# Performance work log

Measured on AMD Instinct MI355X. Metric: run time of the kernel, lower is better.

Reference implementation:

```python
import jax, jax.numpy as jnp
import numpy as np

N_NODES = 10000
N_EDGES = 80000
OBS_DIMS = 128
HIDDEN = 1024
ACT_DIMS = 8
N_GRAPHS = 64


def setup_inputs() -> dict:
    key = jax.random.key(0)
    ks = jax.random.split(key, 8)
    x = jax.random.normal(ks[0], (N_NODES, OBS_DIMS), dtype=jnp.float32)
    edge_index = jax.random.randint(ks[1], (2, N_EDGES), 0, N_NODES, dtype=jnp.int64)
    batch = jnp.sort(jax.random.randint(ks[2], (N_NODES,), 0, N_GRAPHS, dtype=jnp.int64))
    # Glorot-style init for weights, zero bias (as in PyG GCNConv / Linear defaults)
    W1 = jax.random.normal(ks[3], (OBS_DIMS, HIDDEN), dtype=jnp.float32) * (1.0 / np.sqrt(OBS_DIMS))
    b1 = jnp.zeros((HIDDEN,), dtype=jnp.float32)
    W2 = jax.random.normal(ks[4], (HIDDEN, HIDDEN), dtype=jnp.float32) * (1.0 / np.sqrt(HIDDEN))
    b2 = jnp.zeros((HIDDEN,), dtype=jnp.float32)
    Wl = jax.random.normal(ks[5], (HIDDEN, ACT_DIMS), dtype=jnp.float32) * (1.0 / np.sqrt(HIDDEN))
    bl = jnp.zeros((ACT_DIMS,), dtype=jnp.float32)
    return {"x": x, "edge_index": edge_index, "batch": batch,
            "W1": W1, "b1": b1, "W2": W2, "b2": b2, "Wl": Wl, "bl": bl}


def _gcn_conv(x, src, dst, dinv, W, b, n):
    """PyG GCNConv: D^-1/2 (A+I) D^-1/2 X W + b (self-loops already in src/dst)."""
    h = x @ W                                   # [N, out]
    norm = (dinv[src] * dinv[dst])[:, None]      # [E+N, 1]
    msg = h[src] * norm                          # gather + scale
    out = jax.ops.segment_sum(msg, dst, num_segments=n)
    return out + b


def reference(x, edge_index, batch, W1, b1, W2, b2, Wl, bl):
    n = x.shape[0]
    loops = jnp.arange(n, dtype=edge_index.dtype)
    src = jnp.concatenate([edge_index[0], loops])  # add self-loops
    dst = jnp.concatenate([edge_index[1], loops])
    # degree (with self-loops) from destination column, as PyG does
    deg = jax.ops.segment_sum(jnp.ones_like(dst, dtype=x.dtype), dst, num_segments=n)
    dinv = jax.lax.rsqrt(jnp.maximum(deg, 1.0))

    h = jax.nn.relu(_gcn_conv(x, src, dst, dinv, W1, b1, n))
    h = _gcn_conv(h, src, dst, dinv, W2, b2, n)
    h = jnp.tanh(h @ Wl + bl)                    # [N, act_dims]

    # global_mean_pool over batch segment ids
    sums = jax.ops.segment_sum(h, batch, num_segments=N_GRAPHS)
    counts = jax.ops.segment_sum(jnp.ones((n, 1), h.dtype), batch, num_segments=N_GRAPHS)
    return sums / jnp.maximum(counts, 1.0)       # [N_GRAPHS, act_dims]
```

## Files before the change

kernel.cpp:

```cpp
#include <hip/hip_runtime.h>
#include <hip/hip_bf16.h>

#define NNODES 10000
#define NEDGES 80000
#define OBS    128
#define HID    1024
#define ACTD   8
#define NGR    64
#define CAP    32

typedef __bf16 bf16x8 __attribute__((ext_vector_type(8)));
typedef float  f32x4  __attribute__((ext_vector_type(4)));
typedef ushort us8    __attribute__((ext_vector_type(8)));
typedef const __attribute__((address_space(1))) unsigned int gl_u32;
typedef __attribute__((address_space(3))) unsigned int lds_u32;

__device__ __forceinline__ ushort f2b(float f) {
    union { float f; unsigned int i; } v; v.f = f;
    unsigned int lsb = (v.i >> 16) & 1u;
    unsigned int r = v.i + 0x7fffu + lsb;
    return (ushort)(r >> 16);
}
__device__ __forceinline__ int cix(int v, int hi) {
    return v < 0 ? 0 : (v >= hi ? hi - 1 : v);
}

__global__ __launch_bounds__(256) void k_fill(const int* __restrict__ src,
                                              const int* __restrict__ dst,
                                              const int* __restrict__ batch,
                                              int* __restrict__ deg,
                                              int* __restrict__ cntg,
                                              ushort* __restrict__ esrc,
                                              float* __restrict__ zacc,
                                              float* __restrict__ out) {
    __shared__ int lh[NGR];
    int t = threadIdx.x;
    int idx = blockIdx.x * 256 + t;
    if (t < NGR) lh[t] = 0;
    if (idx < NNODES * ACTD) zacc[idx] = 0.0f;
    if (idx < NGR * ACTD) out[idx] = 0.0f;
    if (idx < NEDGES) {
        int s = cix(src[idx], NNODES), d = cix(dst[idx], NNODES);
        int pos = atomicAdd(&deg[d], 1);
        if (pos < CAP) esrc[(size_t)d * CAP + pos] = (ushort)s;
    }
    __syncthreads();
    if (idx < NNODES) atomicAdd(&lh[cix(batch[idx], NGR)], 1);
    __syncthreads();
    if (t < NGR) {
        int c = lh[t];
        if (c) atomicAdd(&cntg[t], c);
    }
}

__global__ __launch_bounds__(256) void k_prepagg(const float* __restrict__ x,
                                                 const int* __restrict__ deg,
                                                 const ushort* __restrict__ esrc,
                                                 ushort* __restrict__ aggbf,
                                                 const float* __restrict__ W1,
                                                 const float* __restrict__ W2,
                                                 const float* __restrict__ Wl,
                                                 const float* __restrict__ b2,
                                                 const float* __restrict__ bl,
                                                 ushort* __restrict__ Wt1,
                                                 ushort* __restrict__ M2bf,
                                                 float* __restrict__ b2l) {
    int blk = blockIdx.x;
    int t = threadIdx.x;
    if (blk < 2500) {
        int wv = (blk * 256 + t) >> 6;
        int lane = t & 63;
        if (wv >= NNODES) return;
        int q = lane >> 4, c = lane & 15;
        int dg = deg[wv];
        float dd = rsqrtf((float)(dg + 1));
        float4 v0 = make_float4(0.f, 0.f, 0.f, 0.f), v1 = v0;
        if (q == 0) {
            const float* xs = x + (size_t)wv * OBS + c * 8;
            float4 a0 = *(const float4*)(xs);
            float4 a1 = *(const float4*)(xs + 4);
            v0.x = a0.x * dd; v0.y = a0.y * dd; v0.z = a0.z * dd; v0.w = a0.w * dd;
            v1.x = a1.x * dd; v1.y = a1.y * dd; v1.z = a1.z * dd; v1.w = a1.w * dd;
        }
        int dcl = dg < CAP ? dg : CAP;
        const ushort* bkt = esrc + (size_t)wv * CAP;
        for (int e = q; e < dcl; e += 4) {
            int s = bkt[e];
            float w = rsqrtf((float)(deg[s] + 1));
            const float* xs = x + (size_t)s * OBS + c * 8;
            float4 a0 = *(const float4*)(xs);
            float4 a1 = *(const float4*)(xs + 4);
            v0.x += a0.x * w; v0.y += a0.y * w; v0.z += a0.z * w; v0.w += a0.w * w;
            v1.x += a1.x * w; v1.y += a1.y * w; v1.z += a1.z * w; v1.w += a1.w * w;
        }
        #pragma unroll
        for (int off = 16; off <= 32; off <<= 1) {
            v0.x += __shfl_xor(v0.x, off); v0.y += __shfl_xor(v0.y, off);
            v0.z += __shfl_xor(v0.z, off); v0.w += __shfl_xor(v0.w, off);
            v1.x += __shfl_xor(v1.x, off); v1.y += __shfl_xor(v1.y, off);
            v1.z += __shfl_xor(v1.z, off); v1.w += __shfl_xor(v1.w, off);
        }
        if (q == 0) {
            us8 o;
            o[0] = f2b(v0.x * dd); o[1] = f2b(v0.y * dd); o[2] = f2b(v0.z * dd); o[3] = f2b(v0.w * dd);
            o[4] = f2b(v1.x * dd); o[5] = f2b(v1.y * dd); o[6] = f2b(v1.z * dd); o[7] = f2b(v1.w * dd);
            *(us8*)(aggbf + (size_t)wv * OBS + c * 8) = o;
        }
        return;
    }
    if (blk < 3525) {
        __shared__ float part[4][8];
        int r = blk - 2500;
        int lane = t & 63, w = t >> 6;
        const float* wrow = (r == HID) ? b2 : (W2 + (size_t)r * HID);
        float4 a = *((const float4*)wrow + t);
        float av[4] = {a.x, a.y, a.z, a.w};
        float acc[ACTD];
        #pragma unroll
        for (int j = 0; j < ACTD; ++j) acc[j] = 0.0f;
        #pragma unroll
        for (int kk = 0; kk < 4; ++kk) {
            int k = t * 4 + kk;
            float4 w0 = *(const float4*)(Wl + (size_t)k * ACTD);
            float4 w1 = *(const float4*)(Wl + (size_t)k * ACTD + 4);
            float av_k = av[kk];
            acc[0] += av_k * w0.x; acc[1] += av_k * w0.y;
            acc[2] += av_k * w0.z; acc[3] += av_k * w0.w;
            acc[4] += av_k * w1.x; acc[5] += av_k * w1.y;
            acc[6] += av_k * w1.z; acc[7] += av_k * w1.w;
        }
        #pragma unroll
        for (int off = 32; off > 0; off >>= 1)
            #pragma unroll
            for (int j = 0; j < ACTD; ++j)
                acc[j] += __shfl_down(acc[j], off);
        if (lane == 0)
            #pragma unroll
            for (int j = 0; j < ACTD; ++j) part[w][j] = acc[j];
        __syncthreads();
        if (t < ACTD) {
            float m = part[0][t] + part[1][t] + part[2][t] + part[3][t];
            if (r == HID) b2l[t] = m + bl[t];
            else          M2bf[r * ACTD + t] = f2b(m);
        }
        return;
    }
    __shared__ float tile[32][33];
    int tb = blk - 3525;
    int bx = (tb & 31) * 32, by = (tb >> 5) * 32;
    int tx = t & 31, ty = t >> 5;
    #pragma unroll
    for (int i = 0; i < 32; i += 8)
        tile[ty + i][tx] = W1[(size_t)(by + ty + i) * HID + bx + tx];
    __syncthreads();
    #pragma unroll
    for (int i = 0; i < 32; i += 8)
        Wt1[(size_t)(bx + ty + i) * OBS + by + tx] = f2b(tile[tx][ty + i]);
}

__global__ __launch_bounds__(256) void k_gemm1_fused(const ushort* __restrict__ A,
                                                     const ushort* __restrict__ Bt,
                                                     const float* __restrict__ bias,
                                                     const ushort* __restrict__ M2bf,
                                                     float* __restrict__ zacc,
                                                     int M) {
    __shared__ ushort buf[128 * 136 + 16 * 128];
    ushort* As    = buf;
    ushort* Bs    = buf + 8192;
    ushort* stage = buf;
    ushort* M2t   = buf + 128 * 136;

    const int t = threadIdx.x;
    const int bm = blockIdx.x, bn = blockIdx.y;
    const int lane = t & 63, wv = t >> 6;
    const int wm = (wv & 1) * 64, wn = (wv >> 1) * 64;
    const int l16 = lane & 15, kg = (lane >> 4) * 8;

    if (t < 128) {
        ushort4 a = *(const ushort4*)(M2bf + (size_t)(bn * 128 + t) * ACTD);
        ushort4 b = *(const ushort4*)(M2bf + (size_t)(bn * 128 + t) * ACTD + 4);
        M2t[0 * 128 + t] = a.x; M2t[1 * 128 + t] = a.y;
        M2t[2 * 128 + t] = a.z; M2t[3 * 128 + t] = a.w;
        M2t[4 * 128 + t] = b.x; M2t[5 * 128 + t] = b.y;
        M2t[6 * 128 + t] = b.z; M2t[7 * 128 + t] = b.w;
        #pragma unroll
        for (int j = 8; j < 16; ++j) M2t[j * 128 + t] = 0;
    }

    f32x4 acc[4][4];
    #pragma unroll
    for (int i = 0; i < 4; ++i)
        #pragma unroll
        for (int j = 0; j < 4; ++j)
            acc[i][j] = (f32x4){0.f, 0.f, 0.f, 0.f};

    const int rs = t >> 3;
    const int cs = (t & 7) * 8;
    #pragma unroll
    for (int kt = 0; kt < OBS; kt += 64) {
        #pragma unroll
        for (int p = 0; p < 4; ++p) {
            int r = rs + p * 32;
            int gr = bm * 128 + r; if (gr >= M) gr = M - 1;
            __builtin_amdgcn_global_load_lds(
                (gl_u32*)(A + (size_t)gr * OBS + kt + cs),
                (lds_u32*)(As + r * 64 + cs), 16, 0, 0);
            int gn = bn * 128 + r;
            __builtin_amdgcn_global_load_lds(
                (gl_u32*)(Bt + (size_t)gn * OBS + kt + cs),
                (lds_u32*)(Bs + r * 64 + cs), 16, 0, 0);
        }
        __syncthreads();
        #pragma unroll
        for (int k2 = 0; k2 < 64; k2 += 32) {
            bf16x8 af[4], bfr[4];
            #pragma unroll
            for (int i = 0; i < 4; ++i)
                af[i] = *(const bf16x8*)(As + (wm + i * 16 + l16) * 64 + k2 + kg);
            #pragma unroll
            for (int j = 0; j < 4; ++j)
                bfr[j] = *(const bf16x8*)(Bs + (wn + j * 16 + l16) * 64 + k2 + kg);
            #pragma unroll
            for (int i = 0; i < 4; ++i)
                #pragma unroll
                for (int j = 0; j < 4; ++j)
                    acc[i][j] = __builtin_amdgcn_mfma_f32_16x16x32_bf16(af[i], bfr[j], acc[i][j], 0, 0, 0);
        }
        __syncthreads();
    }

    #pragma unroll
    for (int i = 0; i < 4; ++i) {
        int rowb = wm + i * 16 + (lane >> 4) * 4;
        #pragma unroll
        for (int j = 0; j < 4; ++j) {
            int col = wn + j * 16 + l16;
            float bj = bias[bn * 128 + col];
            #pragma unroll
            for (int r = 0; r < 4; ++r)
                stage[(rowb + r) * 136 + col] = f2b(fmaxf(acc[i][j][r] + bj, 0.0f));
        }
    }
    __syncthreads();

    #pragma unroll
    for (int st = 0; st < 2; ++st) {
        int row0 = wv * 32 + st * 16;
        f32x4 z = (f32x4){0.f, 0.f, 0.f, 0.f};
        #pragma unroll
        for (int kt = 0; kt < 128; kt += 32) {
            bf16x8 a = *(const bf16x8*)(stage + (row0 + l16) * 136 + kt + kg);
            bf16x8 b = *(const bf16x8*)(M2t + l16 * 128 + kt + kg);
            z = __builtin_amdgcn_mfma_f32_16x16x32_bf16(a, b, z, 0, 0, 0);
        }
        if (l16 < ACTD) {
            int rowb = bm * 128 + row0 + (lane >> 4) * 4;
            #pragma unroll
            for (int r = 0; r < 4; ++r)
                if (rowb + r < M)
                    atomicAdd(&zacc[(size_t)(rowb + r) * ACTD + l16], z[r]);
        }
    }
}

__global__ __launch_bounds__(256) void k_zfinal(const float* __restrict__ zacc,
                                                const int* __restrict__ deg,
                                                const ushort* __restrict__ esrc,
                                                const float* __restrict__ b2l,
                                                const int* __restrict__ batch,
                                                const int* __restrict__ cntg,
                                                float* __restrict__ out, int n) {
    __shared__ float part[NGR * ACTD];
    int t = threadIdx.x;
    part[t] = 0.0f; part[t + 256] = 0.0f;
    __syncthreads();

    int idx = blockIdx.x * 256 + t;
    int i = idx >> 3, j = idx & 7;
    if (i < n) {
        int dg = deg[i];
        float dd = rsqrtf((float)(dg + 1));
        float v = dd * zacc[idx];
        int dcl = dg < CAP ? dg : CAP;
        const ushort* bkt = esrc + (size_t)i * CAP;
        for (int e = 0; e < dcl; ++e) {
            int s = bkt[e];
            float w = rsqrtf((float)(deg[s] + 1));
            v += w * zacc[(size_t)s * ACTD + j];
        }
        v *= dd;
        int g = cix(batch[i], NGR);
        int c = cntg[g];
        float invc = 1.0f / (float)(c > 0 ? c : 1);
        float tz = tanhf(v + b2l[j]) * invc;
        atomicAdd(&part[g * ACTD + j], tz);
    }
    __syncthreads();

    int i0 = (blockIdx.x * 256) >> 3;
    int i1 = (blockIdx.x * 256 + 255) >> 3;
    if (i0 >= n) return;
    if (i1 >= n) i1 = n - 1;
    int g0 = cix(batch[i0], NGR), g1 = cix(batch[i1], NGR);
    int ng = g1 - g0 + 1;
    for (int u = t; u < ng * ACTD; u += 256)
        atomicAdd(&out[g0 * ACTD + u], part[g0 * ACTD + u]);
}

extern "C" void kernel_launch(void* const* d_in, const int* in_sizes, int n_in,
                              void* d_out, int out_size, void* d_ws, size_t ws_size,
                              hipStream_t stream) {
    const float* x   = (const float*)d_in[0];
    const int*   ei  = (const int*)d_in[1];
    const int*   bat = (const int*)d_in[2];
    const float* W1  = (const float*)d_in[3];
    const float* b1  = (const float*)d_in[4];
    const float* W2  = (const float*)d_in[5];
    const float* b2v = (const float*)d_in[6];
    const float* Wl  = (const float*)d_in[7];
    const float* bl  = (const float*)d_in[8];
    float* out = (float*)d_out;

    const int N = NNODES, E = NEDGES;
    const int* src = ei;
    const int* dst = ei + E;

    char* ws = (char*)d_ws;
    size_t off = 0;
    int*    deg    = (int*)(ws + off);   off += 40192;
    int*    cntg   = (int*)(ws + off);   off += 256;
    float*  b2l    = (float*)(ws + off); off += 256;
    ushort* M2bf   = (ushort*)(ws + off); off += (size_t)HID * ACTD * 2;
    ushort* Wt1    = (ushort*)(ws + off); off += (size_t)HID * OBS * 2;
    float*  zacc   = (float*)(ws + off); off += (size_t)N * ACTD * 4;
    ushort* aggbf  = (ushort*)(ws + off); off += (size_t)N * OBS * 2;
    ushort* esrc   = (ushort*)(ws + off); off += (size_t)N * CAP * 2;

    hipMemsetAsync(deg, 0, 40448, stream);

    k_fill<<<313, 256, 0, stream>>>(src, dst, bat, deg, cntg, esrc, zacc, out);

    k_prepagg<<<3653, 256, 0, stream>>>(x, deg, esrc, aggbf,
                                        W1, W2, Wl, b2v, bl, Wt1, M2bf, b2l);

    k_gemm1_fused<<<dim3((N + 127) / 128, HID / 128), 256, 0, stream>>>(
        aggbf, Wt1, b1, M2bf, zacc, N);

    k_zfinal<<<(N * ACTD + 255) / 256, 256, 0, stream>>>(
        zacc, deg, esrc, b2l, bat, cntg, out, N);
}
```

Before: 113.2 us.

## Regroup launches: fuse weight prep into fill kernel, split aggregation, add ILP

```diff
diff --git a/kernel.cpp b/kernel.cpp
--- a/kernel.cpp
+++ b/kernel.cpp
@@ -25,92 +25,47 @@
     return v < 0 ? 0 : (v >= hi ? hi - 1 : v);
 }
 
-__global__ __launch_bounds__(256) void k_fill(const int* __restrict__ src,
-                                              const int* __restrict__ dst,
-                                              const int* __restrict__ batch,
-                                              int* __restrict__ deg,
-                                              int* __restrict__ cntg,
-                                              ushort* __restrict__ esrc,
-                                              float* __restrict__ zacc,
-                                              float* __restrict__ out) {
-    __shared__ int lh[NGR];
-    int t = threadIdx.x;
-    int idx = blockIdx.x * 256 + t;
-    if (t < NGR) lh[t] = 0;
-    if (idx < NNODES * ACTD) zacc[idx] = 0.0f;
-    if (idx < NGR * ACTD) out[idx] = 0.0f;
-    if (idx < NEDGES) {
-        int s = cix(src[idx], NNODES), d = cix(dst[idx], NNODES);
-        int pos = atomicAdd(&deg[d], 1);
-        if (pos < CAP) esrc[(size_t)d * CAP + pos] = (ushort)s;
-    }
-    __syncthreads();
-    if (idx < NNODES) atomicAdd(&lh[cix(batch[idx], NGR)], 1);
-    __syncthreads();
-    if (t < NGR) {
-        int c = lh[t];
-        if (c) atomicAdd(&cntg[t], c);
-    }
-}
-
-__global__ __launch_bounds__(256) void k_prepagg(const float* __restrict__ x,
-                                                 const int* __restrict__ deg,
-                                                 const ushort* __restrict__ esrc,
-                                                 ushort* __restrict__ aggbf,
-                                                 const float* __restrict__ W1,
-                                                 const float* __restrict__ W2,
-                                                 const float* __restrict__ Wl,
-                                                 const float* __restrict__ b2,
-                                                 const float* __restrict__ bl,
-                                                 ushort* __restrict__ Wt1,
-                                                 ushort* __restrict__ M2bf,
-                                                 float* __restrict__ b2l) {
+__global__ __launch_bounds__(256) void k_fillprep(const int* __restrict__ src,
+                                                  const int* __restrict__ dst,
+                                                  const int* __restrict__ batch,
+                                                  int* __restrict__ deg,
+                                                  int* __restrict__ cntg,
+                                                  ushort* __restrict__ esrc,
+                                                  float* __restrict__ zacc,
+                                                  float* __restrict__ out,
+                                                  const float* __restrict__ W1,
+                                                  const float* __restrict__ W2,
+                                                  const float* __restrict__ Wl,
+                                                  const float* __restrict__ b2,
+                                                  const float* __restrict__ bl,
+                                                  ushort* __restrict__ Wt1,
+                                                  ushort* __restrict__ M2bf,
+                                                  float* __restrict__ b2l) {
     int blk = blockIdx.x;
     int t = threadIdx.x;
-    if (blk < 2500) {
-        int wv = (blk * 256 + t) >> 6;
-        int lane = t & 63;
-        if (wv >= NNODES) return;
-        int q = lane >> 4, c = lane & 15;
-        int dg = deg[wv];
-        float dd = rsqrtf((float)(dg + 1));
-        float4 v0 = make_float4(0.f, 0.f, 0.f, 0.f), v1 = v0;
-        if (q == 0) {
-            const float* xs = x + (size_t)wv * OBS + c * 8;
-            float4 a0 = *(const float4*)(xs);
-            float4 a1 = *(const float4*)(xs + 4);
-            v0.x = a0.x * dd; v0.y = a0.y * dd; v0.z = a0.z * dd; v0.w = a0.w * dd;
-            v1.x = a1.x * dd; v1.y = a1.y * dd; v1.z = a1.z * dd; v1.w = a1.w * dd;
-        }
-        int dcl = dg < CAP ? dg : CAP;
-        const ushort* bkt = esrc + (size_t)wv * CAP;
-        for (int e = q; e < dcl; e += 4) {
-            int s = bkt[e];
-            float w = rsqrtf((float)(deg[s] + 1));
-            const float* xs = x + (size_t)s * OBS + c * 8;
-            float4 a0 = *(const float4*)(xs);
-            float4 a1 = *(const float4*)(xs + 4);
-            v0.x += a0.x * w; v0.y += a0.y * w; v0.z += a0.z * w; v0.w += a0.w * w;
-            v1.x += a1.x * w; v1.y += a1.y * w; v1.z += a1.z * w; v1.w += a1.w * w;
-        }
-        #pragma unroll
-        for (int off = 16; off <= 32; off <<= 1) {
-            v0.x += __shfl_xor(v0.x, off); v0.y += __shfl_xor(v0.y, off);
-            v0.z += __shfl_xor(v0.z, off); v0.w += __shfl_xor(v0.w, off);
-            v1.x += __shfl_xor(v1.x, off); v1.y += __shfl_xor(v1.y, off);
-            v1.z += __shfl_xor(v1.z, off); v1.w += __shfl_xor(v1.w, off);
-        }
-        if (q == 0) {
-            us8 o;
-            o[0] = f2b(v0.x * dd); o[1] = f2b(v0.y * dd); o[2] = f2b(v0.z * dd); o[3] = f2b(v0.w * dd);
-            o[4] = f2b(v1.x * dd); o[5] = f2b(v1.y * dd); o[6] = f2b(v1.z * dd); o[7] = f2b(v1.w * dd);
-            *(us8*)(aggbf + (size_t)wv * OBS + c * 8) = o;
+    if (blk < 313) {
+        __shared__ int lh[NGR];
+        int idx = blk * 256 + t;
+        if (t < NGR) lh[t] = 0;
+        if (idx < NNODES * ACTD) zacc[idx] = 0.0f;
+        if (idx < NGR * ACTD) out[idx] = 0.0f;
+        if (idx < NEDGES) {
+            int s = cix(src[idx], NNODES), d = cix(dst[idx], NNODES);
+            int pos = atomicAdd(&deg[d], 1);
+            if (pos < CAP) esrc[(size_t)d * CAP + pos] = (ushort)s;
+        }
+        __syncthreads();
+        if (idx < NNODES) atomicAdd(&lh[cix(batch[idx], NGR)], 1);
+        __syncthreads();
+        if (t < NGR) {
+            int c = lh[t];
+            if (c) atomicAdd(&cntg[t], c);
         }
         return;
     }
-    if (blk < 3525) {
+    if (blk < 1338) {
         __shared__ float part[4][8];
-        int r = blk - 2500;
+        int r = blk - 313;
         int lane = t & 63, w = t >> 6;
         const float* wrow = (r == HID) ? b2 : (W2 + (size_t)r * HID);
         float4 a = *((const float4*)wrow + t);
@@ -146,7 +101,7 @@
         return;
     }
     __shared__ float tile[32][33];
-    int tb = blk - 3525;
+    int tb = blk - 1338;
     int bx = (tb & 31) * 32, by = (tb >> 5) * 32;
     int tx = t & 31, ty = t >> 5;
     #pragma unroll
@@ -156,6 +111,51 @@
     #pragma unroll
     for (int i = 0; i < 32; i += 8)
         Wt1[(size_t)(bx + ty + i) * OBS + by + tx] = f2b(tile[tx][ty + i]);
+}
+
+__global__ void k_aggx(const float* __restrict__ x, const int* __restrict__ deg,
+                       const ushort* __restrict__ esrc, ushort* __restrict__ aggbf, int n) {
+    int wv = (blockIdx.x * 256 + threadIdx.x) >> 6;
+    int lane = threadIdx.x & 63;
+    if (wv >= n) return;
+    int q = lane >> 4, c = lane & 15;
+    int dg = deg[wv];
+    float dd = rsqrtf((float)(dg + 1));
+    float4 v0 = make_float4(0.f, 0.f, 0.f, 0.f), v1 = v0;
+    if (q == 0) {
+        const float* xs = x + (size_t)wv * OBS + c * 8;
+        float4 a0 = *(const float4*)(xs);
+        float4 a1 = *(const float4*)(xs + 4);
+        v0.x = a0.x * dd; v0.y = a0.y * dd; v0.z = a0.z * dd; v0.w = a0.w * dd;
+        v1.x = a1.x * dd; v1.y = a1.y * dd; v1.z = a1.z * dd; v1.w = a1.w * dd;
+    }
+    int dcl = dg < CAP ? dg : CAP;
+    const ushort* bkt = esrc + (size_t)wv * CAP;
+    int e = q;
+    int s_next = (e < dcl) ? (int)bkt[e] : 0;
+    for (; e < dcl; e += 4) {
+        int s = s_next;
+        s_next = (e + 4 < dcl) ? (int)bkt[e + 4] : 0;
+        float w = rsqrtf((float)(deg[s] + 1));
+        const float* xs = x + (size_t)s * OBS + c * 8;
+        float4 a0 = *(const float4*)(xs);
+        float4 a1 = *(const float4*)(xs + 4);
+        v0.x += a0.x * w; v0.y += a0.y * w; v0.z += a0.z * w; v0.w += a0.w * w;
+        v1.x += a1.x * w; v1.y += a1.y * w; v1.z += a1.z * w; v1.w += a1.w * w;
+    }
+    #pragma unroll
+    for (int off = 16; off <= 32; off <<= 1) {
+        v0.x += __shfl_xor(v0.x, off); v0.y += __shfl_xor(v0.y, off);
+        v0.z += __shfl_xor(v0.z, off); v0.w += __shfl_xor(v0.w, off);
+        v1.x += __shfl_xor(v1.x, off); v1.y += __shfl_xor(v1.y, off);
+        v1.z += __shfl_xor(v1.z, off); v1.w += __shfl_xor(v1.w, off);
+    }
+    if (q == 0) {
+        us8 o;
+        o[0] = f2b(v0.x * dd); o[1] = f2b(v0.y * dd); o[2] = f2b(v0.z * dd); o[3] = f2b(v0.w * dd);
+        o[4] = f2b(v1.x * dd); o[5] = f2b(v1.y * dd); o[6] = f2b(v1.z * dd); o[7] = f2b(v1.w * dd);
+        *(us8*)(aggbf + (size_t)wv * OBS + c * 8) = o;
+    }
 }
 
 __global__ __launch_bounds__(256) void k_gemm1_fused(const ushort* __restrict__ A,
@@ -280,15 +280,23 @@
     if (i < n) {
         int dg = deg[i];
         float dd = rsqrtf((float)(dg + 1));
-        float v = dd * zacc[idx];
+        float va = dd * zacc[idx], vb = 0.0f;
         int dcl = dg < CAP ? dg : CAP;
         const ushort* bkt = esrc + (size_t)i * CAP;
-        for (int e = 0; e < dcl; ++e) {
-            int s = bkt[e];
-            float w = rsqrtf((float)(deg[s] + 1));
-            v += w * zacc[(size_t)s * ACTD + j];
-        }
-        v *= dd;
+        int e = 0;
+        for (; e + 2 <= dcl; e += 2) {
+            int s0 = bkt[e], s1 = bkt[e + 1];
+            int d0 = deg[s0], d1 = deg[s1];
+            float z0 = zacc[(size_t)s0 * ACTD + j];
+            float z1 = zacc[(size_t)s1 * ACTD + j];
+            va += rsqrtf((float)(d0 + 1)) * z0;
+            vb += rsqrtf((float)(d1 + 1)) * z1;
+        }
+        if (e < dcl) {
+            int s0 = bkt[e];
+            va += rsqrtf((float)(deg[s0] + 1)) * zacc[(size_t)s0 * ACTD + j];
+        }
+        float v = (va + vb) * dd;
         int g = cix(batch[i], NGR);
         int c = cntg[g];
         float invc = 1.0f / (float)(c > 0 ? c : 1);
@@ -338,10 +346,10 @@
 
     hipMemsetAsync(deg, 0, 40448, stream);
 
-    k_fill<<<313, 256, 0, stream>>>(src, dst, bat, deg, cntg, esrc, zacc, out);
-
-    k_prepagg<<<3653, 256, 0, stream>>>(x, deg, esrc, aggbf,
-                                        W1, W2, Wl, b2v, bl, Wt1, M2bf, b2l);
+    k_fillprep<<<1466, 256, 0, stream>>>(src, dst, bat, deg, cntg, esrc, zacc, out,
+                                         W1, W2, Wl, b2v, bl, Wt1, M2bf, b2l);
+
+    k_aggx<<<(N * 64 + 255) / 256, 256, 0, stream>>>(x, deg, esrc, aggbf, N);
 
     k_gemm1_fused<<<dim3((N + 127) / 128, HID / 128), 256, 0, stream>>>(
         aggbf, Wt1, b1, M2bf, zacc, N);
```

Result: no change. 113.5 us (+0.2%).
